# Optimization experiments

Hardware: AMD Instinct MI355X
Metric: run time of the kernel (lower is better)

Reference implementation:

```python
import jax, jax.numpy as jnp
import numpy as np

N_NODES = 50000
N_EDGES = 1600000
F_IN = 256
HID = 256
HEADS = 8
HD = HID // HEADS  # 32
SLOPE = 0.2
EPS = 1e-5


def setup_inputs() -> dict:
    key = jax.random.key(0)
    ks = jax.random.split(key, 10)
    node_features = jax.random.normal(ks[0], (N_NODES, F_IN), jnp.float32)
    edge_index = jax.random.randint(ks[1], (2, N_EDGES), 0, N_NODES, jnp.int32)
    s = 1.0 / np.sqrt(F_IN)
    W = jax.random.uniform(ks[2], (HEADS, F_IN, HD), jnp.float32, -s, s)
    bw = jax.random.uniform(ks[3], (HEADS, HD), jnp.float32, -s, s)
    sa = 1.0 / np.sqrt(2 * HD)
    A = jax.random.uniform(ks[4], (HEADS, 2 * HD), jnp.float32, -sa, sa)
    ba = jax.random.uniform(ks[5], (HEADS,), jnp.float32, -sa, sa)
    gamma = jnp.ones((HEADS, HD), jnp.float32)
    beta = jnp.zeros((HEADS, HD), jnp.float32)
    so = 1.0 / np.sqrt(HD)
    Wout = jax.random.uniform(ks[6], (HD, HID), jnp.float32, -so, so)
    bout = jax.random.uniform(ks[7], (HID,), jnp.float32, -so, so)
    return dict(node_features=node_features, edge_index=edge_index, W=W, bw=bw,
                A=A, ba=ba, gamma=gamma, beta=beta, Wout=Wout, bout=bout)


def _head(x, W, bw, a, ba, gamma, beta, tgt, src):
    h = x @ W + bw                         # [N, d]
    # attn(concat(h_i, h_j)) = h_i @ a1 + h_j @ a2 + ba  (linear over concat)
    si = h @ a[:HD]                        # [N]
    sj = h @ a[HD:]                        # [N]
    e = si[tgt] + sj[src] + ba             # [E]
    e = jnp.where(e >= 0, e, SLOPE * e)    # leaky_relu
    # scatter_softmax over edges grouped by target node (stable)
    m = jax.ops.segment_max(e, tgt, num_segments=N_NODES)
    ex = jnp.exp(e - m[tgt])
    den = jax.ops.segment_sum(ex, tgt, num_segments=N_NODES)
    alpha = ex / den[tgt]                  # [E]  (dropout in eval mode = identity)
    msg = alpha[:, None] * h[src]          # [E, d]
    agg = jax.ops.segment_sum(msg, tgt, num_segments=N_NODES)  # [N, d]
    out = agg + h                          # skip connection
    out = jnp.where(out > 0, out, jnp.expm1(out))  # ELU
    mu = out.mean(axis=-1, keepdims=True)
    var = out.var(axis=-1, keepdims=True)
    return (out - mu) * jax.lax.rsqrt(var + EPS) * gamma + beta


def reference(node_features, edge_index, W, bw, A, ba, gamma, beta, Wout, bout):
    tgt = edge_index[0]
    src = edge_index[1]
    heads = jax.vmap(_head, in_axes=(None, 0, 0, 0, 0, 0, 0, None, None))(
        node_features, W, bw, A, ba, gamma, beta, tgt, src)   # [H, N, d]
    mean = heads.mean(axis=0)                                  # [N, d]
    y = mean @ Wout + bout                                     # [N, HID]
    return jnp.where(y > 0, y, jnp.expm1(y))                   # ELU
```

## Files before the change

kernel.cpp:

```cpp
#include <hip/hip_runtime.h>
#include <hip/hip_bf16.h>
#include <hip/hip_fp16.h>

#define N_NODES 50000
#define N_EDGES 1600000
#define HEADS 8
#define HD 32
#define FIN 256
#define HID 256

typedef unsigned short u16;
typedef unsigned int u32;

typedef short s8v __attribute__((ext_vector_type(8)));
typedef float f4v __attribute__((ext_vector_type(4)));

__device__ __forceinline__ u32 pk2(float lo, float hi) {
  __hip_bfloat162 b = __float22bfloat162_rn(make_float2(lo, hi));
  union { __hip_bfloat162 b2; u32 u; } c;
  c.b2 = b;
  return c.u;
}

__global__ __launch_bounds__(256) void k_gemm(
    const float* __restrict__ X, const float* __restrict__ W,
    const float* __restrict__ bw, const float* __restrict__ A,
    __half* __restrict__ Hb, float* __restrict__ si, float* __restrict__ sj) {
  __shared__ __align__(16) u16 Xs[128 * 40];
  __shared__ __align__(16) u16 Wt[128 * 40];

  const int t = threadIdx.x;
  const int m0 = (blockIdx.x >> 1) * 128;
  const int n0 = (blockIdx.x & 1) * 128;
  const int w = t >> 6;
  const int lane = t & 63;
  const int l15 = lane & 15;
  const int quad = lane >> 4;
  const int wm = (w >> 1) * 64;
  const int wn = (w & 1) * 64;

  f4v acc[4][4];
#pragma unroll
  for (int i = 0; i < 4; i++)
#pragma unroll
    for (int j = 0; j < 4; j++) acc[i][j] = (f4v){0.f, 0.f, 0.f, 0.f};

  const int nl = t & 127;
  const int half = t >> 7;
  const int gn = n0 + nl;
  const int gh = gn >> 5, gd = gn & 31;

  for (int k0 = 0; k0 < FIN; k0 += 32) {
#pragma unroll
    for (int p = 0; p < 4; p++) {
      int row = p * 32 + (t >> 3);
      int f4 = t & 7;
      int node = m0 + row;
      float4 xv = make_float4(0.f, 0.f, 0.f, 0.f);
      if (node < N_NODES) xv = *(const float4*)&X[node * FIN + k0 + f4 * 4];
      u32* dst = (u32*)&Xs[row * 40 + f4 * 4];
      dst[0] = pk2(xv.x, xv.y);
      dst[1] = pk2(xv.z, xv.w);
    }
    {
      const float* wp = W + gh * (FIN * HD) + (k0 + half * 16) * HD + gd;
#pragma unroll
      for (int j = 0; j < 8; j++) {
        float lo = wp[(2 * j) * HD];
        float hi = wp[(2 * j + 1) * HD];
        *(u32*)&Wt[nl * 40 + half * 16 + 2 * j] = pk2(lo, hi);
      }
    }
    __syncthreads();
    s8v af[4], bf[4];
#pragma unroll
    for (int mi = 0; mi < 4; mi++)
      af[mi] = *(const s8v*)&Xs[(wm + mi * 16 + l15) * 40 + quad * 8];
#pragma unroll
    for (int ni = 0; ni < 4; ni++)
      bf[ni] = *(const s8v*)&Wt[(wn + ni * 16 + l15) * 40 + quad * 8];
#pragma unroll
    for (int mi = 0; mi < 4; mi++)
#pragma unroll
      for (int ni = 0; ni < 4; ni++)
        acc[mi][ni] = __builtin_amdgcn_mfma_f32_16x16x32_bf16(af[mi], bf[ni], acc[mi][ni], 0, 0, 0);
    __syncthreads();
  }

  const int head0 = (n0 + wn) >> 5;
  const int head1 = head0 + 1;
  float c1a0 = A[head0 * 64 + l15],      c1a1 = A[head0 * 64 + 16 + l15];
  float c2a0 = A[head0 * 64 + 32 + l15], c2a1 = A[head0 * 64 + 48 + l15];
  float c1b0 = A[head1 * 64 + l15],      c1b1 = A[head1 * 64 + 16 + l15];
  float c2b0 = A[head1 * 64 + 32 + l15], c2b1 = A[head1 * 64 + 48 + l15];

#pragma unroll
  for (int mi = 0; mi < 4; mi++) {
#pragma unroll
    for (int ni = 0; ni < 4; ni++) {
      float b = bw[n0 + wn + ni * 16 + l15];
#pragma unroll
      for (int r = 0; r < 4; r++) acc[mi][ni][r] += b;
    }
    const int rbase = m0 + wm + mi * 16 + quad * 4;
#pragma unroll
    for (int r = 0; r < 4; r++) {
      int node = rbase + r;
      if (node < N_NODES) {
#pragma unroll
        for (int ni = 0; ni < 4; ni++) {
          int col = n0 + wn + ni * 16 + l15;
          Hb[node * HID + col] = __float2half_rn(acc[mi][ni][r]);
        }
      }
    }
    float s1a[4], s2a[4], s1b[4], s2b[4];
#pragma unroll
    for (int r = 0; r < 4; r++) {
      s1a[r] = acc[mi][0][r] * c1a0 + acc[mi][1][r] * c1a1;
      s2a[r] = acc[mi][0][r] * c2a0 + acc[mi][1][r] * c2a1;
      s1b[r] = acc[mi][2][r] * c1b0 + acc[mi][3][r] * c1b1;
      s2b[r] = acc[mi][2][r] * c2b0 + acc[mi][3][r] * c2b1;
    }
#pragma unroll
    for (int off = 1; off <= 8; off <<= 1) {
#pragma unroll
      for (int r = 0; r < 4; r++) {
        s1a[r] += __shfl_xor(s1a[r], off);
        s2a[r] += __shfl_xor(s2a[r], off);
        s1b[r] += __shfl_xor(s1b[r], off);
        s2b[r] += __shfl_xor(s2b[r], off);
      }
    }
    if (l15 == 0) {
#pragma unroll
      for (int r = 0; r < 4; r++) {
        int node = rbase + r;
        if (node < N_NODES) {
          si[node * HEADS + head0] = s1a[r];
          sj[node * HEADS + head0] = s2a[r];
          si[node * HEADS + head1] = s1b[r];
          sj[node * HEADS + head1] = s2b[r];
        }
      }
    }
  }
}

__global__ void k_hist(const int* __restrict__ tgt, int* __restrict__ cnt) {
  int e = blockIdx.x * 256 + threadIdx.x;
  if (e < N_EDGES) atomicAdd(&cnt[tgt[e]], 1);
}

__global__ __launch_bounds__(256) void k_scan1(const int* __restrict__ cnt,
    int* __restrict__ excl, int* __restrict__ bsum) {
  __shared__ int s[256];
  const int t = threadIdx.x;
  const int i = blockIdx.x * 256 + t;
  int v = (i < N_NODES) ? cnt[i] : 0;
  s[t] = v;
  __syncthreads();
  int x = v;
  for (int off = 1; off < 256; off <<= 1) {
    int y = (t >= off) ? s[t - off] : 0;
    __syncthreads();
    x += y;
    s[t] = x;
    __syncthreads();
  }
  if (i < N_NODES) excl[i] = x - v;
  if (t == 255) bsum[blockIdx.x] = x;
}

__global__ __launch_bounds__(256) void k_scan2(const int* __restrict__ bsum,
                                               int* __restrict__ boff) {
  __shared__ int s[256];
  const int t = threadIdx.x;
  int v = (t < 196) ? bsum[t] : 0;
  s[t] = v;
  __syncthreads();
  int x = v;
  for (int off = 1; off < 256; off <<= 1) {
    int y = (t >= off) ? s[t - off] : 0;
    __syncthreads();
    x += y;
    s[t] = x;
    __syncthreads();
  }
  if (t < 196) boff[t] = x - v;
}

__global__ void k_scan3(const int* __restrict__ excl, const int* __restrict__ boff,
                        int* __restrict__ rowptr, int* __restrict__ cursor) {
  int i = blockIdx.x * 256 + threadIdx.x;
  if (i < N_NODES) {
    int v = excl[i] + boff[blockIdx.x];
    rowptr[i] = v;
    cursor[i] = v;
  }
}

__global__ void k_scatter(const int* __restrict__ tgt, const int* __restrict__ src,
                          int* __restrict__ cursor, int* __restrict__ sortedSrc) {
  int e = blockIdx.x * 256 + threadIdx.x;
  if (e < N_EDGES) {
    int tg = tgt[e];
    int pos = atomicAdd(&cursor[tg], 1);
    sortedSrc[pos] = src[e];
  }
}

__global__ __launch_bounds__(256) void k_fused(
    const __half* __restrict__ Hb, const float* __restrict__ si,
    const float* __restrict__ sj, const float* __restrict__ ba,
    const float* __restrict__ gamma, const float* __restrict__ beta,
    const float* __restrict__ Wout, const float* __restrict__ bout,
    const int* __restrict__ rowptr, const int* __restrict__ cnt,
    const int* __restrict__ sortedSrc, float* __restrict__ out) {
  __shared__ float accsT[8][8][33];
  __shared__ float dens[8][32];
  __shared__ float lnorm[256];
  __shared__ __align__(16) float meanv[32];

  const int n = blockIdx.x;
  const int t = threadIdx.x;
  const int cg = t & 31;
  const int es = t >> 5;
  const int hh = cg >> 2;
  const int start = rowptr[n];
  const int deg = cnt[n];

  const float sb = si[n * HEADS + hh] + ba[hh];
  const char* hbBase = (const char*)Hb + 16 * cg;
  const int* ss = sortedSrc + start;

  float acc[8] = {0.f, 0.f, 0.f, 0.f, 0.f, 0.f, 0.f, 0.f};
  float den = 0.f;
#pragma unroll 4
  for (int slot = es; slot < deg; slot += 8) {
    int s = ss[slot];
    float e = sb + sj[s * HEADS + hh];
    e = (e >= 0.f) ? e : 0.2f * e;
    float exv = __expf(e);
    float4 hb4 = *(const float4*)(hbBase + (size_t)s * (HID * 2));
    const __half2* hp = (const __half2*)&hb4;
#pragma unroll
    for (int d = 0; d < 4; d++) {
      acc[2 * d]     += exv * __low2float(hp[d]);
      acc[2 * d + 1] += exv * __high2float(hp[d]);
    }
    den += exv;
  }

#pragma unroll
  for (int j = 0; j < 8; j++) accsT[j][es][cg] = acc[j];
  dens[es][cg] = den;
  __syncthreads();

  float accT = 0.f, denT = 0.f;
#pragma unroll
  for (int e2 = 0; e2 < 8; e2++) {
    accT += accsT[t & 7][e2][t >> 3];
    denT += dens[e2][t >> 3];
  }
  float hs = __half2float(Hb[n * HID + t]);
  float v = ((deg > 0) ? __fdividef(accT, denT) : 0.f) + hs;
  v = (v > 0.f) ? v : (__expf(v) - 1.f);
  float sum = v, sq = v * v;
#pragma unroll
  for (int off = 16; off >= 1; off >>= 1) {
    sum += __shfl_xor(sum, off);
    sq  += __shfl_xor(sq, off);
  }
  float mu = sum * (1.f / 32.f);
  float var = sq * (1.f / 32.f) - mu * mu;
  float nv = (v - mu) * rsqrtf(var + 1e-5f) * gamma[t] + beta[t];
  lnorm[t] = nv;
  __syncthreads();
  if (t < 32) {
    float m2 = 0.f;
#pragma unroll
    for (int h2 = 0; h2 < HEADS; h2++) m2 += lnorm[h2 * 32 + t];
    meanv[t] = m2 * 0.125f;
  }
  __syncthreads();
  float y = bout[t];
#pragma unroll
  for (int k = 0; k < 32; k++) y += meanv[k] * Wout[k * HID + t];
  y = (y > 0.f) ? y : (__expf(y) - 1.f);
  out[n * HID + t] = y;
}

extern "C" void kernel_launch(void* const* d_in, const int* in_sizes, int n_in,
                              void* d_out, int out_size, void* d_ws, size_t ws_size,
                              hipStream_t stream) {
  const float* X     = (const float*)d_in[0];
  const int*   EI    = (const int*)d_in[1];
  const float* W     = (const float*)d_in[2];
  const float* bw    = (const float*)d_in[3];
  const float* A     = (const float*)d_in[4];
  const float* ba    = (const float*)d_in[5];
  const float* gamma = (const float*)d_in[6];
  const float* beta  = (const float*)d_in[7];
  const float* Wout  = (const float*)d_in[8];
  const float* bout  = (const float*)d_in[9];
  float* out = (float*)d_out;
  const int* tgt = EI;
  const int* src = EI + N_EDGES;

  char* ws = (char*)d_ws;
  size_t off = 0;
  auto alloc = [&](size_t bytes) -> void* {
    void* p = ws + off;
    off += bytes;
    off = (off + 255) & ~(size_t)255;
    return p;
  };
  __half* Hb       = (__half*)alloc((size_t)N_NODES * HID * 2);
  float* si        = (float*)alloc((size_t)N_NODES * HEADS * 4);
  float* sj        = (float*)alloc((size_t)N_NODES * HEADS * 4);
  int*   cnt       = (int*)  alloc((size_t)N_NODES * 4);
  int*   excl      = (int*)  alloc((size_t)N_NODES * 4);
  int*   bsum      = (int*)  alloc(256 * 4);
  int*   boff      = (int*)  alloc(256 * 4);
  int*   rowptr    = (int*)  alloc((size_t)N_NODES * 4);
  int*   cursor    = (int*)  alloc((size_t)N_NODES * 4);
  int*   sortedSrc = (int*)  alloc((size_t)N_EDGES * 4);

  hipMemsetAsync(cnt, 0, (size_t)N_NODES * 4, stream);
  k_hist<<<(N_EDGES + 255) / 256, 256, 0, stream>>>(tgt, cnt);
  k_scan1<<<196, 256, 0, stream>>>(cnt, excl, bsum);
  k_scan2<<<1, 256, 0, stream>>>(bsum, boff);
  k_scan3<<<196, 256, 0, stream>>>(excl, boff, rowptr, cursor);
  k_scatter<<<(N_EDGES + 255) / 256, 256, 0, stream>>>(tgt, src, cursor, sortedSrc);
  k_gemm<<<((N_NODES + 127) / 128) * 2, 256, 0, stream>>>(X, W, bw, A, Hb, si, sj);
  k_fused<<<N_NODES, 256, 0, stream>>>(Hb, si, sj, ba, gamma, beta, Wout, bout,
                                       rowptr, cnt, sortedSrc, out);
}
```

Baseline: 523.1 us.

## Map one node per wavefront in fused kernel and widen GEMM tile to full width

The fused aggregation kernel now handles one node per 64-lane wavefront instead of one per 256-thread block. Reductions that went through shared memory and block barriers become wave shuffles, and the output projection is vectorised with float4 stores. The GEMM now computes all 256 output columns per 512-thread block, so each X tile is read and converted once rather than twice, and X is loaded with nontemporal hints. Each wave now walks a node's edges with only two edge streams, which lowers per-node parallelism for high-degree nodes and could expose gather latency.

```diff
diff --git a/kernel.cpp b/kernel.cpp
--- a/kernel.cpp
+++ b/kernel.cpp
@@ -14,6 +14,7 @@
 
 typedef short s8v __attribute__((ext_vector_type(8)));
 typedef float f4v __attribute__((ext_vector_type(4)));
+typedef float fx4 __attribute__((ext_vector_type(4)));
 
 __device__ __forceinline__ u32 pk2(float lo, float hi) {
   __hip_bfloat162 b = __float22bfloat162_rn(make_float2(lo, hi));
@@ -22,22 +23,21 @@
   return c.u;
 }
 
-__global__ __launch_bounds__(256) void k_gemm(
+__global__ __launch_bounds__(512) void k_gemm(
     const float* __restrict__ X, const float* __restrict__ W,
     const float* __restrict__ bw, const float* __restrict__ A,
     __half* __restrict__ Hb, float* __restrict__ si, float* __restrict__ sj) {
   __shared__ __align__(16) u16 Xs[128 * 40];
-  __shared__ __align__(16) u16 Wt[128 * 40];
+  __shared__ __align__(16) u16 Wt[256 * 40];
 
   const int t = threadIdx.x;
-  const int m0 = (blockIdx.x >> 1) * 128;
-  const int n0 = (blockIdx.x & 1) * 128;
+  const int m0 = blockIdx.x * 128;
   const int w = t >> 6;
   const int lane = t & 63;
   const int l15 = lane & 15;
   const int quad = lane >> 4;
-  const int wm = (w >> 1) * 64;
-  const int wn = (w & 1) * 64;
+  const int wm = (w >> 2) * 64;
+  const int wn = (w & 3) * 64;
 
   f4v acc[4][4];
 #pragma unroll
@@ -45,22 +45,22 @@
 #pragma unroll
     for (int j = 0; j < 4; j++) acc[i][j] = (f4v){0.f, 0.f, 0.f, 0.f};
 
-  const int nl = t & 127;
-  const int half = t >> 7;
-  const int gn = n0 + nl;
-  const int gh = gn >> 5, gd = gn & 31;
+  const int nl = t & 255;
+  const int half = t >> 8;
+  const int gh = nl >> 5, gd = nl & 31;
 
   for (int k0 = 0; k0 < FIN; k0 += 32) {
 #pragma unroll
-    for (int p = 0; p < 4; p++) {
-      int row = p * 32 + (t >> 3);
+    for (int p = 0; p < 2; p++) {
+      int row = p * 64 + (t >> 3);
       int f4 = t & 7;
       int node = m0 + row;
-      float4 xv = make_float4(0.f, 0.f, 0.f, 0.f);
-      if (node < N_NODES) xv = *(const float4*)&X[node * FIN + k0 + f4 * 4];
+      fx4 xv = (fx4){0.f, 0.f, 0.f, 0.f};
+      if (node < N_NODES)
+        xv = __builtin_nontemporal_load((const fx4*)&X[node * FIN + k0 + f4 * 4]);
       u32* dst = (u32*)&Xs[row * 40 + f4 * 4];
-      dst[0] = pk2(xv.x, xv.y);
-      dst[1] = pk2(xv.z, xv.w);
+      dst[0] = pk2(xv[0], xv[1]);
+      dst[1] = pk2(xv[2], xv[3]);
     }
     {
       const float* wp = W + gh * (FIN * HD) + (k0 + half * 16) * HD + gd;
@@ -87,7 +87,7 @@
     __syncthreads();
   }
 
-  const int head0 = (n0 + wn) >> 5;
+  const int head0 = wn >> 5;
   const int head1 = head0 + 1;
   float c1a0 = A[head0 * 64 + l15],      c1a1 = A[head0 * 64 + 16 + l15];
   float c2a0 = A[head0 * 64 + 32 + l15], c2a1 = A[head0 * 64 + 48 + l15];
@@ -98,7 +98,7 @@
   for (int mi = 0; mi < 4; mi++) {
 #pragma unroll
     for (int ni = 0; ni < 4; ni++) {
-      float b = bw[n0 + wn + ni * 16 + l15];
+      float b = bw[wn + ni * 16 + l15];
 #pragma unroll
       for (int r = 0; r < 4; r++) acc[mi][ni][r] += b;
     }
@@ -109,7 +109,7 @@
       if (node < N_NODES) {
 #pragma unroll
         for (int ni = 0; ni < 4; ni++) {
-          int col = n0 + wn + ni * 16 + l15;
+          int col = wn + ni * 16 + l15;
           Hb[node * HID + col] = __float2half_rn(acc[mi][ni][r]);
         }
       }
@@ -217,15 +217,11 @@
     const float* __restrict__ Wout, const float* __restrict__ bout,
     const int* __restrict__ rowptr, const int* __restrict__ cnt,
     const int* __restrict__ sortedSrc, float* __restrict__ out) {
-  __shared__ float accsT[8][8][33];
-  __shared__ float dens[8][32];
-  __shared__ float lnorm[256];
-  __shared__ __align__(16) float meanv[32];
-
-  const int n = blockIdx.x;
   const int t = threadIdx.x;
-  const int cg = t & 31;
-  const int es = t >> 5;
+  const int lane = t & 63;
+  const int n = blockIdx.x * 4 + (t >> 6);
+  const int cg = lane & 31;
+  const int es = lane >> 5;
   const int hh = cg >> 2;
   const int start = rowptr[n];
   const int deg = cnt[n];
@@ -237,8 +233,8 @@
   float acc[8] = {0.f, 0.f, 0.f, 0.f, 0.f, 0.f, 0.f, 0.f};
   float den = 0.f;
 #pragma unroll 4
-  for (int slot = es; slot < deg; slot += 8) {
-    int s = ss[slot];
+  for (int slot = es; slot < deg; slot += 2) {
+    int s = __builtin_nontemporal_load(ss + slot);
     float e = sb + sj[s * HEADS + hh];
     e = (e >= 0.f) ? e : 0.2f * e;
     float exv = __expf(e);
@@ -251,44 +247,61 @@
     }
     den += exv;
   }
-
-#pragma unroll
-  for (int j = 0; j < 8; j++) accsT[j][es][cg] = acc[j];
-  dens[es][cg] = den;
-  __syncthreads();
-
-  float accT = 0.f, denT = 0.f;
-#pragma unroll
-  for (int e2 = 0; e2 < 8; e2++) {
-    accT += accsT[t & 7][e2][t >> 3];
-    denT += dens[e2][t >> 3];
-  }
-  float hs = __half2float(Hb[n * HID + t]);
-  float v = ((deg > 0) ? __fdividef(accT, denT) : 0.f) + hs;
-  v = (v > 0.f) ? v : (__expf(v) - 1.f);
-  float sum = v, sq = v * v;
-#pragma unroll
-  for (int off = 16; off >= 1; off >>= 1) {
-    sum += __shfl_xor(sum, off);
-    sq  += __shfl_xor(sq, off);
-  }
+#pragma unroll
+  for (int j = 0; j < 8; j++) acc[j] += __shfl_xor(acc[j], 32);
+  den += __shfl_xor(den, 32);
+
+  float4 h4 = *(const float4*)((const char*)Hb + (size_t)n * (HID * 2) + 16 * cg);
+  const __half2* hq = (const __half2*)&h4;
+  float inv = (deg > 0) ? __fdividef(1.f, den) : 0.f;
+  float v[8], sum = 0.f, sq = 0.f;
+#pragma unroll
+  for (int j = 0; j < 8; j++) {
+    float hv = (j & 1) ? __high2float(hq[j >> 1]) : __low2float(hq[j >> 1]);
+    float x = acc[j] * inv + hv;
+    x = (x > 0.f) ? x : (__expf(x) - 1.f);
+    v[j] = x;
+    sum += x;
+    sq += x * x;
+  }
+  sum += __shfl_xor(sum, 1); sq += __shfl_xor(sq, 1);
+  sum += __shfl_xor(sum, 2); sq += __shfl_xor(sq, 2);
   float mu = sum * (1.f / 32.f);
   float var = sq * (1.f / 32.f) - mu * mu;
-  float nv = (v - mu) * rsqrtf(var + 1e-5f) * gamma[t] + beta[t];
-  lnorm[t] = nv;
-  __syncthreads();
-  if (t < 32) {
-    float m2 = 0.f;
-#pragma unroll
-    for (int h2 = 0; h2 < HEADS; h2++) m2 += lnorm[h2 * 32 + t];
-    meanv[t] = m2 * 0.125f;
-  }
-  __syncthreads();
-  float y = bout[t];
-#pragma unroll
-  for (int k = 0; k < 32; k++) y += meanv[k] * Wout[k * HID + t];
-  y = (y > 0.f) ? y : (__expf(y) - 1.f);
-  out[n * HID + t] = y;
+  float rstd = rsqrtf(var + 1e-5f);
+  fx4 g0 = *(const fx4*)&gamma[cg * 8];
+  fx4 g1 = *(const fx4*)&gamma[cg * 8 + 4];
+  fx4 b0 = *(const fx4*)&beta[cg * 8];
+  fx4 b1 = *(const fx4*)&beta[cg * 8 + 4];
+  float m2[8];
+#pragma unroll
+  for (int j = 0; j < 8; j++) {
+    float g = (j < 4) ? g0[j] : g1[j - 4];
+    float bb = (j < 4) ? b0[j] : b1[j - 4];
+    m2[j] = (v[j] - mu) * rstd * g + bb;
+  }
+#pragma unroll
+  for (int j = 0; j < 8; j++) {
+    m2[j] += __shfl_xor(m2[j], 4);
+    m2[j] += __shfl_xor(m2[j], 8);
+    m2[j] += __shfl_xor(m2[j], 16);
+  }
+
+  fx4 y = *(const fx4*)&bout[4 * lane];
+#pragma unroll
+  for (int q = 0; q < 4; q++) {
+    float mv[8];
+#pragma unroll
+    for (int j = 0; j < 8; j++) mv[j] = __shfl(m2[j], q) * 0.125f;
+#pragma unroll
+    for (int j = 0; j < 8; j++) {
+      fx4 w4 = *(const fx4*)&Wout[(q * 8 + j) * HID + 4 * lane];
+      y += mv[j] * w4;
+    }
+  }
+#pragma unroll
+  for (int c = 0; c < 4; c++) y[c] = (y[c] > 0.f) ? y[c] : (__expf(y[c]) - 1.f);
+  __builtin_nontemporal_store(y, (fx4*)&out[(size_t)n * HID + 4 * lane]);
 }
 
 extern "C" void kernel_launch(void* const* d_in, const int* in_sizes, int n_in,
@@ -333,7 +346,8 @@
   k_scan2<<<1, 256, 0, stream>>>(bsum, boff);
   k_scan3<<<196, 256, 0, stream>>>(excl, boff, rowptr, cursor);
   k_scatter<<<(N_EDGES + 255) / 256, 256, 0, stream>>>(tgt, src, cursor, sortedSrc);
-  k_gemm<<<((N_NODES + 127) / 128) * 2, 256, 0, stream>>>(X, W, bw, A, Hb, si, sj);
-  k_fused<<<N_NODES, 256, 0, stream>>>(Hb, si, sj, ba, gamma, beta, Wout, bout,
-                                       rowptr, cnt, sortedSrc, out);
-}
+  k_gemm<<<(N_NODES + 127) / 128, 512, 0, stream>>>(X, W, bw, A, Hb, si, sj);
+  k_fused<<<(N_NODES + 3) / 4, 256, 0, stream>>>(Hb, si, sj, ba, gamma, beta,
+                                                 Wout, bout, rowptr, cnt,
+                                                 sortedSrc, out);
+}
```

New measurement: 495.9 us. 1.05x faster.
